# Performance work log

Measured on AMD Instinct MI355X. Metric: run time of the kernel, lower is better.

The kernel has to match this reference:

```python
import jax, jax.numpy as jnp
import numpy as np
from jax import lax
from jax.scipy.special import logsumexp

B, S, H, T, V = 64, 512, 768, 16, 30522


def setup_inputs() -> dict:
    key = jax.random.key(0)
    ks = jax.random.split(key, 8)
    src = jax.random.randint(ks[0], (B, S), 0, V, dtype=jnp.int32)
    label = jax.random.randint(ks[1], (B, S), 0, T, dtype=jnp.int32)
    padding_mask = jnp.ones((B, S), jnp.int32)
    emb_table = jax.random.normal(ks[2], (V, H), jnp.float32) * 0.02
    W = jax.random.normal(ks[3], (H, T), jnp.float32) * 0.02
    b = jnp.zeros((T,), jnp.float32)
    start_trans = jax.random.normal(ks[4], (T,), jnp.float32) * 0.1
    end_trans = jax.random.normal(ks[5], (T,), jnp.float32) * 0.1
    transitions = jax.random.normal(ks[6], (T, T), jnp.float32) * 0.1
    return dict(src=src, label=label, padding_mask=padding_mask,
                emb_table=emb_table, W=W, b=b, start_trans=start_trans,
                end_trans=end_trans, transitions=transitions)


def crf_log_likelihood(emissions, tags, mask, start_trans, end_trans, transitions):
    # emissions [S,B,T], tags [S,B] int, mask [S,B] float. torchcrf reduction='sum'.
    nS, nB, nT = emissions.shape
    barange = jnp.arange(nB)
    # --- numerator: score of the gold path ---
    score0 = start_trans[tags[0]] + emissions[0, barange, tags[0]]
    def num_step(score, xs):
        em_t, tag_prev, tag_t, m = xs
        s = transitions[tag_prev, tag_t] + em_t[barange, tag_t]
        return score + s * m, None
    num, _ = lax.scan(num_step, score0, (emissions[1:], tags[:-1], tags[1:], mask[1:]))
    seq_len = jnp.sum(mask, axis=0).astype(jnp.int32)          # [B]
    last_tags = tags[seq_len - 1, barange]
    num = num + end_trans[last_tags]
    # --- denominator: forward algorithm (per-step logsumexp) ---
    alpha0 = start_trans[None, :] + emissions[0]               # [B,T]
    def den_step(alpha, xs):
        em_t, m = xs
        nxt = logsumexp(alpha[:, :, None] + transitions[None, :, :] + em_t[:, None, :], axis=1)
        return jnp.where(m[:, None] > 0, nxt, alpha), None
    alpha, _ = lax.scan(den_step, alpha0, (emissions[1:], mask[1:]))
    den = logsumexp(alpha + end_trans[None, :], axis=1)
    return jnp.sum(num - den)


def viterbi_decode(emissions, start_trans, end_trans, transitions):
    # emissions [S,B,T]; full-length decode (no mask, as in the original call).
    score0 = start_trans[None, :] + emissions[0]               # [B,T]
    def fwd_step(score, em_t):
        br = score[:, :, None] + transitions[None, :, :] + em_t[:, None, :]  # [B,T,T]
        return jnp.max(br, axis=1), jnp.argmax(br, axis=1)
    score, hist = lax.scan(fwd_step, score0, emissions[1:])    # hist [S-1,B,T]
    last = jnp.argmax(score + end_trans[None, :], axis=1)      # [B]
    def back_step(tag, h_t):
        prev = jnp.take_along_axis(h_t, tag[:, None], axis=1)[:, 0]
        return prev, prev
    _, prevs = lax.scan(back_step, last, hist, reverse=True)   # prevs[t] = tag at t
    return jnp.concatenate([prevs, last[None, :]], axis=0)     # [S,B]


def reference(src, label, padding_mask, emb_table, W, b, start_trans, end_trans, transitions):
    bs = src.shape[0]
    emb = emb_table[src]                                       # [B,S,H]
    logits = jnp.einsum('bsh,ht->bst', emb, W) + b             # [B,S,T] (dropout in eval = identity)
    emissions = jnp.transpose(logits, (1, 0, 2))               # [S,B,T]
    tags = label.T                                             # [S,B]
    mask = padding_mask.T.astype(logits.dtype)                 # [S,B]
    ll = crf_log_likelihood(emissions, tags, mask, start_trans, end_trans, transitions)
    loss = -ll / bs
    predict = viterbi_decode(emissions, start_trans, end_trans, transitions).T  # [B,S]
    label_flat = label.reshape(-1)
    pred_flat = predict.reshape(-1).astype(label_flat.dtype)
    label_mask = (label_flat > 0).astype(label_flat.dtype)
    pred_flat = pred_flat * label_mask
    correct = jnp.sum((pred_flat == label_flat).astype(jnp.float32))
    return loss, correct, pred_flat, label_flat
```

## Files before the change

kernel.cpp:

```cpp
#include <hip/hip_runtime.h>

#define Bq 64
#define Sq 512
#define Hq 768
#define Tq 16
#define Vq 30522
#define EMP 516
#define WLP 20

typedef unsigned int u32;
typedef unsigned long long u64;
typedef unsigned char u8;

__device__ __forceinline__ float bperm_f(float v, int byteidx) {
    return __int_as_float(__builtin_amdgcn_ds_bpermute(byteidx, __float_as_int(v)));
}
template <int CTRL>
__device__ __forceinline__ int dpp_i(int v) {
    return __builtin_amdgcn_mov_dpp(v, CTRL, 0xF, 0xF, true);
}
template <int CTRL>
__device__ __forceinline__ float dpp_f(float v) {
    return __int_as_float(dpp_i<CTRL>(__float_as_int(v)));
}

#define QX1 0xB1
#define QX2 0x4E
#define QX3 0x1B
#define RR4  0x124
#define RR8  0x128
#define RR12 0x12C

__device__ __forceinline__ u32 packnib(u32 d) {
    u32 y = d | (d >> 4);
    y &= 0x00FF00FFu;
    y = (y | (y >> 8)) & 0xFFFFu;
    return y;
}
__device__ __forceinline__ u32 nib64(u64 f, u32 s) {
    return ((u32)(f >> (s << 2))) & 15u;
}

__global__ __launch_bounds__(256, 2) void k_table(const float* __restrict__ emb,
                                                  const float* __restrict__ W,
                                                  const float* __restrict__ bias,
                                                  float* __restrict__ table,
                                                  float* __restrict__ out) {
    if (blockIdx.x == 0 && threadIdx.x == 0) out[1] = 0.0f;
    __shared__ float WL[Hq * WLP];
    const int tid = threadIdx.x;

    #pragma unroll
    for (int k = 0; k < 12; ++k) {
        int idx = tid + (k << 8);
        float4 v = *reinterpret_cast<const float4*>(W + idx * 4);
        *reinterpret_cast<float4*>(&WL[(idx >> 2) * WLP + ((idx & 3) << 2)]) = v;
    }
    __syncthreads();

    const int r_loc = tid >> 2;
    const int q     = tid & 3;
    const int v     = blockIdx.x * 64 + r_loc;
    const int vc    = v < Vq ? v : Vq - 1;
    const float* arow = emb + (size_t)vc * Hq;

    float acc[16];
    #pragma unroll
    for (int t = 0; t < 16; ++t) acc[t] = 0.0f;

    float4 buf[8];
    #pragma unroll
    for (int u = 0; u < 8; ++u)
        buf[u] = *reinterpret_cast<const float4*>(arow + (q + 4 * u) * 4);

    for (int k6 = 0; k6 < 6; ++k6) {
        #pragma unroll
        for (int u = 0; u < 8; ++u) {
            const int k = k6 * 8 + u;
            float4 av = buf[u];
            if (k + 8 < 48)
                buf[u] = *reinterpret_cast<const float4*>(arow + (q + 4 * (k + 8)) * 4);
            const int hb = (q + 4 * k) * 4;
            #pragma unroll
            for (int a = 0; a < 4; ++a) {
                float s = (a == 0) ? av.x : (a == 1) ? av.y : (a == 2) ? av.z : av.w;
                const float* wr = &WL[(hb + a) * WLP];
                float4 w0 = *reinterpret_cast<const float4*>(wr);
                float4 w1 = *reinterpret_cast<const float4*>(wr + 4);
                float4 w2 = *reinterpret_cast<const float4*>(wr + 8);
                float4 w3 = *reinterpret_cast<const float4*>(wr + 12);
                acc[0]  = fmaf(s, w0.x, acc[0]);
                acc[1]  = fmaf(s, w0.y, acc[1]);
                acc[2]  = fmaf(s, w0.z, acc[2]);
                acc[3]  = fmaf(s, w0.w, acc[3]);
                acc[4]  = fmaf(s, w1.x, acc[4]);
                acc[5]  = fmaf(s, w1.y, acc[5]);
                acc[6]  = fmaf(s, w1.z, acc[6]);
                acc[7]  = fmaf(s, w1.w, acc[7]);
                acc[8]  = fmaf(s, w2.x, acc[8]);
                acc[9]  = fmaf(s, w2.y, acc[9]);
                acc[10] = fmaf(s, w2.z, acc[10]);
                acc[11] = fmaf(s, w2.w, acc[11]);
                acc[12] = fmaf(s, w3.x, acc[12]);
                acc[13] = fmaf(s, w3.y, acc[13]);
                acc[14] = fmaf(s, w3.z, acc[14]);
                acc[15] = fmaf(s, w3.w, acc[15]);
            }
        }
    }
    #pragma unroll
    for (int t = 0; t < 16; ++t) {
        acc[t] += dpp_f<QX1>(acc[t]);
        acc[t] += dpp_f<QX2>(acc[t]);
    }
    if (v < Vq) {
        float4 bv = *reinterpret_cast<const float4*>(bias + q * 4);
        float4 o = make_float4(acc[q * 4] + bv.x, acc[q * 4 + 1] + bv.y,
                               acc[q * 4 + 2] + bv.z, acc[q * 4 + 3] + bv.w);
        *reinterpret_cast<float4*>(table + (size_t)v * Tq + q * 4) = o;
    }
}

#define G16_DPP(PV) \
      float r1 = dpp_f<QX1>(PV), r2 = dpp_f<QX2>(PV), r3 = dpp_f<QX3>(PV); \
      float r4 = dpp_f<RR4>(PV), r8v = dpp_f<RR8>(PV), r12v = dpp_f<RR12>(PV); \
      float r5 = dpp_f<QX1>(r4), r6 = dpp_f<QX2>(r4), r7 = dpp_f<QX3>(r4); \
      float r9 = dpp_f<QX1>(r8v), r10 = dpp_f<QX2>(r8v), r11 = dpp_f<QX3>(r8v); \
      float r13 = dpp_f<QX1>(r12v), r14 = dpp_f<QX2>(r12v), r15 = dpp_f<QX3>(r12v);

#define G16_BP(PV) \
      const int rb_ = (lane & 48) << 2; \
      float r1 = bperm_f(PV, rb_ + (pm[1] << 2)),  r2 = bperm_f(PV, rb_ + (pm[2] << 2)); \
      float r3 = bperm_f(PV, rb_ + (pm[3] << 2)),  r4 = bperm_f(PV, rb_ + (pm[4] << 2)); \
      float r5 = bperm_f(PV, rb_ + (pm[5] << 2)),  r6 = bperm_f(PV, rb_ + (pm[6] << 2)); \
      float r7 = bperm_f(PV, rb_ + (pm[7] << 2)),  r8v = bperm_f(PV, rb_ + (pm[8] << 2)); \
      float r9 = bperm_f(PV, rb_ + (pm[9] << 2)),  r10 = bperm_f(PV, rb_ + (pm[10] << 2)); \
      float r11 = bperm_f(PV, rb_ + (pm[11] << 2)), r12v = bperm_f(PV, rb_ + (pm[12] << 2)); \
      float r13 = bperm_f(PV, rb_ + (pm[13] << 2)), r14 = bperm_f(PV, rb_ + (pm[14] << 2)); \
      float r15 = bperm_f(PV, rb_ + (pm[15] << 2));

#define DEN_BODY(ff) \
      float a0 = P * Wt[0];     a0 = fmaf(r1, Wt[1], a0);   a0 = fmaf(r2, Wt[2], a0);   a0 = fmaf(r3, Wt[3], a0); \
      float a1 = r4 * Wt[4];    a1 = fmaf(r5, Wt[5], a1);   a1 = fmaf(r6, Wt[6], a1);   a1 = fmaf(r7, Wt[7], a1); \
      float a2 = r8v * Wt[8];   a2 = fmaf(r9, Wt[9], a2);   a2 = fmaf(r10, Wt[10], a2); a2 = fmaf(r11, Wt[11], a2); \
      float a3 = r12v * Wt[12]; a3 = fmaf(r13, Wt[13], a3); a3 = fmaf(r14, Wt[14], a3); a3 = fmaf(r15, Wt[15], a3); \
      P = ((a0 + a1) + (a2 + a3)) * (ff);

#define DEN_STEP_F(ff) { G16_DPP(P); DEN_BODY(ff) }
#define DEN_STEP_B(ff) { G16_BP(P);  DEN_BODY(ff) }

#define VIT_BODY(emv, tcur) \
      float v0 = P + Wt[0],     v1 = r1 + Wt[1],    v2 = r2 + Wt[2],    v3 = r3 + Wt[3]; \
      float v4 = r4 + Wt[4],    v5 = r5 + Wt[5],    v6 = r6 + Wt[6],    v7 = r7 + Wt[7]; \
      float v8 = r8v + Wt[8],   v9 = r9 + Wt[9],    v10 = r10 + Wt[10], v11 = r11 + Wt[11]; \
      float v12 = r12v + Wt[12], v13 = r13 + Wt[13], v14 = r14 + Wt[14], v15 = r15 + Wt[15]; \
      float ma = fmaxf(fmaxf(v0, v1), v2),  mb = fmaxf(fmaxf(v3, v4), v5); \
      float mc = fmaxf(fmaxf(v6, v7), v8),  md = fmaxf(fmaxf(v9, v10), v11); \
      float me = fmaxf(fmaxf(v12, v13), v14); \
      float mv = fmaxf(fmaxf(fmaxf(ma, mb), mc), fmaxf(fmaxf(md, me), v15)); \
      P = mv + (emv); \
      if (lane < 16) scb[(tcur) * Tq + j] = P;

#define VIT_STEP_F(emv, tcur) { G16_DPP(P); VIT_BODY(emv, tcur) }
#define VIT_STEP_B(emv, tcur) { G16_BP(P);  VIT_BODY(emv, tcur) }

#define SCAN4(STEP, X1, X2, X3) \
      STEP(f0.X1, 1) STEP(f0.X2, 2) STEP(f0.X3, 3) \
      { float4 fc = emrow[1]; \
        for (int t0 = 4; t0 < Sq; t0 += 4) { \
            float4 fn; \
            if (t0 + 4 < Sq) fn = emrow[(t0 >> 2) + 1]; \
            STEP(fc.x, t0) STEP(fc.y, t0 + 1) STEP(fc.z, t0 + 2) STEP(fc.w, t0 + 3) \
            fc = fn; \
        } }

#define DSTEP_F(emv, tcur) DEN_STEP_F(emv)
#define DSTEP_B(emv, tcur) DEN_STEP_B(emv)

__global__ __launch_bounds__(64) void k_scan(const int* __restrict__ src,
                                             const int* __restrict__ label,
                                             const int* __restrict__ pmask,
                                             const float* __restrict__ table,
                                             const float* __restrict__ start_t,
                                             const float* __restrict__ end_t,
                                             const float* __restrict__ trans,
                                             float* __restrict__ nd,
                                             float* __restrict__ out) {
    __shared__ __align__(16) char smem[78848];

    const int lane = threadIdx.x;
    const int j  = lane & 15;
    const int b4 = lane >> 4;
    const bool vit = blockIdx.x >= 32;

    int pm[16];
    bool fast;
    {
        float x = __int_as_float(j);
        G16_DPP(x);
        pm[0] = j;
        pm[1] = __float_as_int(r1);   pm[2] = __float_as_int(r2);   pm[3] = __float_as_int(r3);
        pm[4] = __float_as_int(r4);   pm[5] = __float_as_int(r5);   pm[6] = __float_as_int(r6);
        pm[7] = __float_as_int(r7);   pm[8] = __float_as_int(r8v);  pm[9] = __float_as_int(r9);
        pm[10] = __float_as_int(r10); pm[11] = __float_as_int(r11); pm[12] = __float_as_int(r12v);
        pm[13] = __float_as_int(r13); pm[14] = __float_as_int(r14); pm[15] = __float_as_int(r15);
        u32 cov = 0;
        bool inr = true;
        #pragma unroll
        for (int s = 0; s < 16; ++s) {
            inr = inr && (pm[s] >= 0) && (pm[s] < 16);
            cov |= 1u << (pm[s] & 15);
        }
        fast = (__all((inr && cov == 0xFFFFu) ? 1 : 0) != 0);
        if (!fast) {
            pm[0] = j;
            #pragma unroll
            for (int s = 1; s < 16; ++s) pm[s] = (j + s) & 15;
        }
    }

    if (!vit) {
        float* emT = (float*)smem;
        int* srcl  = (int*)(smem + 66048);
        int* labl  = (int*)(smem + 70144);
        const int bb = blockIdx.x * 2;
        const int bm = b4 & 1;
        const int batch = bb + bm;

        #pragma unroll
        for (int k = 0; k < 16; ++k) {
            int idx = lane + (k << 6);
            int bch = idx >> 9, t = idx & 511;
            srcl[idx] = src[(bb + bch) * Sq + t];
            labl[idx] = label[(bb + bch) * Sq + t];
        }
        __syncthreads();
        #pragma unroll 4
        for (int k = 0; k < 256; ++k) {
            int idx = lane + (k << 6);
            int bch = idx >> 13, rem = idx & 8191;
            int t = rem >> 4, jj = rem & 15;
            emT[(bch * 16 + jj) * EMP + t] =
                __expf(table[(size_t)srcl[(bch << 9) + t] * Tq + jj]) * 0.0625f;
        }
        __syncthreads();

        float Wt[16];
        #pragma unroll
        for (int s = 0; s < 16; ++s) Wt[s] = __expf(trans[pm[s] * Tq + j]);

        const float4* emrow = reinterpret_cast<const float4*>(emT + (bm * 16 + j) * EMP);
        float4 f0 = emrow[0];
        float P = __expf(start_t[j]) * f0.x * 16.0f;
        float* scb = nullptr; (void)scb;

        if (fast) { SCAN4(DSTEP_F, y, z, w) }
        else      { SCAN4(DSTEP_B, y, z, w) }

        float val = P * __expf(end_t[j]);
        val += dpp_f<QX1>(val); val += dpp_f<QX2>(val);
        val += dpp_f<RR4>(val); val += dpp_f<RR8>(val);
        float den = (float)(511.0 * 2.7725887222397811) + __logf(val);

        float numv = 0.0f;
        int sl = 0;
        #pragma unroll
        for (int k = 0; k < 32; ++k) {
            int t = j + (k << 4);
            int tag = labl[(bm << 9) + t];
            int m = pmask[batch * Sq + t];
            sl += m;
            float emtt = table[(size_t)srcl[(bm << 9) + t] * Tq + tag];
            if (t == 0) {
                numv += start_t[tag] + emtt;
            } else {
                int tp = labl[(bm << 9) + t - 1];
                numv += (float)m * (trans[tp * Tq + tag] + emtt);
            }
        }
        numv += dpp_f<QX1>(numv); numv += dpp_f<QX2>(numv);
        numv += dpp_f<RR4>(numv); numv += dpp_f<RR8>(numv);
        sl += dpp_i<QX1>(sl); sl += dpp_i<QX2>(sl);
        sl += dpp_i<RR4>(sl); sl += dpp_i<RR8>(sl);
        if (j == 0 && b4 < 2) {
            int last = labl[(bm << 9) + sl - 1];
            nd[batch] = (numv + end_t[last]) - den;
        }
    } else {
        float* em   = (float*)smem;
        float* scb  = (float*)(smem + 33024);
        u8*  hist   = (u8*)(smem + 65792);
        int* srcl   = (int*)(smem + 73984);
        int* labl   = (int*)(smem + 76032);
        u8*  predi  = (u8*)(smem + 78080);
        const int batch = blockIdx.x - 32;

        #pragma unroll
        for (int k = 0; k < 8; ++k) {
            int t = lane + (k << 6);
            srcl[t] = src[batch * Sq + t];
            labl[t] = label[batch * Sq + t];
        }
        __syncthreads();
        #pragma unroll 4
        for (int k = 0; k < 128; ++k) {
            int idx = lane + (k << 6);
            int t = idx >> 4, jj = idx & 15;
            em[jj * EMP + t] = table[(size_t)srcl[t] * Tq + jj];
        }
        __syncthreads();

        float Wt[16];
        #pragma unroll
        for (int s = 0; s < 16; ++s) Wt[s] = trans[pm[s] * Tq + j];

        const float4* emrow = reinterpret_cast<const float4*>(em + j * EMP);
        float4 f0 = emrow[0];
        float P = start_t[j] + f0.x;
        if (lane < 16) scb[j] = P;

        if (fast) { SCAN4(VIT_STEP_F, y, z, w) }
        else      { SCAN4(VIT_STEP_B, y, z, w) }

        float fv = P + end_t[j];
        int fi = j;
        #pragma unroll
        for (int off = 1; off < 16; off <<= 1) {
            float ov = __shfl_xor(fv, off);
            int oi = __shfl_xor(fi, off);
            bool take = (ov > fv) || (ov == fv && oi < fi);
            fv = take ? ov : fv;
            fi = take ? oi : fi;
        }
        __syncthreads();

        {
            float Tt[16];
            #pragma unroll
            for (int m = 0; m < 16; ++m) Tt[m] = trans[m * Tq + j];
            const int r = b4;
            for (int k = 0; k < 128; ++k) {
                int t = 1 + r + 4 * k;
                if (t < Sq) {
                    const float4* sr = reinterpret_cast<const float4*>(scb + (t - 1) * Tq);
                    float4 s0 = sr[0], s1 = sr[1], s2 = sr[2], s3 = sr[3];
                    float w0 = s0.x + Tt[0],  w1 = s0.y + Tt[1],  w2 = s0.z + Tt[2],  w3 = s0.w + Tt[3];
                    float w4 = s1.x + Tt[4],  w5 = s1.y + Tt[5],  w6 = s1.z + Tt[6],  w7 = s1.w + Tt[7];
                    float w8 = s2.x + Tt[8],  w9 = s2.y + Tt[9],  wA = s2.z + Tt[10], wB = s2.w + Tt[11];
                    float wC = s3.x + Tt[12], wD = s3.y + Tt[13], wE = s3.z + Tt[14], wF = s3.w + Tt[15];
                    float ma = fmaxf(fmaxf(w0, w1), w2),  mb = fmaxf(fmaxf(w3, w4), w5);
                    float mc = fmaxf(fmaxf(w6, w7), w8),  md = fmaxf(fmaxf(w9, wA), wB);
                    float me = fmaxf(fmaxf(wC, wD), wE);
                    float mv = fmaxf(fmaxf(fmaxf(ma, mb), mc), fmaxf(fmaxf(md, me), wF));
                    float y0 = fmaf(mv - w0, 1e30f, 0.0f),  y1 = fmaf(mv - w1, 1e30f, 1.0f);
                    float y2 = fmaf(mv - w2, 1e30f, 2.0f),  y3 = fmaf(mv - w3, 1e30f, 3.0f);
                    float y4 = fmaf(mv - w4, 1e30f, 4.0f),  y5 = fmaf(mv - w5, 1e30f, 5.0f);
                    float y6 = fmaf(mv - w6, 1e30f, 6.0f),  y7 = fmaf(mv - w7, 1e30f, 7.0f);
                    float y8 = fmaf(mv - w8, 1e30f, 8.0f),  y9 = fmaf(mv - w9, 1e30f, 9.0f);
                    float yA = fmaf(mv - wA, 1e30f, 10.0f), yB = fmaf(mv - wB, 1e30f, 11.0f);
                    float yC = fmaf(mv - wC, 1e30f, 12.0f), yD = fmaf(mv - wD, 1e30f, 13.0f);
                    float yE = fmaf(mv - wE, 1e30f, 14.0f), yF = fmaf(mv - wF, 1e30f, 15.0f);
                    float na = fminf(fminf(y0, y1), y2),  nb = fminf(fminf(y3, y4), y5);
                    float nc = fminf(fminf(y6, y7), y8),  nd2 = fminf(fminf(y9, yA), yB);
                    float ne = fminf(fminf(yC, yD), yE);
                    float ym = fminf(fminf(fminf(na, nb), nc), fminf(fminf(nd2, ne), yF));
                    hist[(t - 1) * Tq + j] = (unsigned char)(int)ym;
                }
            }
        }
        if (lane < 16) hist[511 * Tq + lane] = (u8)lane;
        __syncthreads();

        u64 rp[8];
        #pragma unroll
        for (int k = 0; k < 8; ++k) {
            uint4 rw = *reinterpret_cast<const uint4*>(&hist[(lane * 8 + k) * Tq]);
            u32 lo = packnib(rw.x) | (packnib(rw.y) << 16);
            u32 hi = packnib(rw.z) | (packnib(rw.w) << 16);
            rp[k] = (u64)lo | ((u64)hi << 32);
        }
        u64 F = rp[7];
        #pragma unroll
        for (int k = 6; k >= 0; --k) {
            u64 nf = 0;
            #pragma unroll
            for (int e = 0; e < 16; ++e) {
                u32 s = (u32)(F >> (e * 4)) & 15u;
                nf |= ((u64)nib64(rp[k], s)) << (e * 4);
            }
            F = nf;
        }
        u32 Flo = (u32)F, Fhi = (u32)(F >> 32);

        u32 pk[8] = {0, 0, 0, 0, 0, 0, 0, 0};
        u32 E = (u32)__builtin_amdgcn_readlane(fi, 0) & 15u;
        #pragma unroll 64
        for (int c = 63; c >= 0; --c) {
            u64 Fc = ((u64)(u32)__builtin_amdgcn_readlane((int)Fhi, c) << 32)
                   | (u64)(u32)__builtin_amdgcn_readlane((int)Flo, c);
            pk[c >> 3] |= E << ((c & 7) * 4);
            E = nib64(Fc, E);
        }

        u32 a0s = (lane & 8) ? pk[1] : pk[0];
        u32 a1s = (lane & 8) ? pk[3] : pk[2];
        u32 a2s = (lane & 8) ? pk[5] : pk[4];
        u32 a3s = (lane & 8) ? pk[7] : pk[6];
        u32 b0s = (lane & 16) ? a1s : a0s;
        u32 b1s = (lane & 16) ? a3s : a2s;
        u32 c0s = (lane & 32) ? b1s : b0s;
        u32 cur = (c0s >> ((lane & 7) * 4)) & 15u;
        u32 w0 = 0, w1 = 0;
        #pragma unroll
        for (int k = 7; k >= 0; --k) {
            cur = nib64(rp[k], cur);
            if (k >= 4) w1 |= cur << ((k - 4) * 8);
            else        w0 |= cur << (k * 8);
        }
        *reinterpret_cast<uint2*>(&predi[lane * 8]) = make_uint2(w0, w1);
        __syncthreads();

        int cnt = 0;
        #pragma unroll
        for (int k = 0; k < 8; ++k) {
            int s_ = lane + (k << 6);
            int lab = labl[s_];
            int pr = (int)predi[s_];
            int mpr = lab > 0 ? pr : 0;
            out[2 + batch * Sq + s_] = (float)mpr;
            out[2 + Bq * Sq + batch * Sq + s_] = (float)lab;
            cnt += (mpr == lab) ? 1 : 0;
        }
        #pragma unroll
        for (int off = 1; off < 64; off <<= 1) cnt += __shfl_xor(cnt, off);
        if (lane == 0) atomicAdd(out + 1, (float)cnt);
    }
}

__global__ __launch_bounds__(64) void k_final(const float* __restrict__ nd,
                                              float* __restrict__ out) {
    float v = nd[threadIdx.x];
    #pragma unroll
    for (int off = 1; off < 64; off <<= 1) v += __shfl_xor(v, off);
    if (threadIdx.x == 0) out[0] = -v * (1.0f / (float)Bq);
}

extern "C" void kernel_launch(void* const* d_in, const int* in_sizes, int n_in,
                              void* d_out, int out_size, void* d_ws, size_t ws_size,
                              hipStream_t stream) {
    const int*   src   = (const int*)d_in[0];
    const int*   label = (const int*)d_in[1];
    const int*   pmask = (const int*)d_in[2];
    const float* emb   = (const float*)d_in[3];
    const float* W     = (const float*)d_in[4];
    const float* bias  = (const float*)d_in[5];
    const float* st    = (const float*)d_in[6];
    const float* en    = (const float*)d_in[7];
    const float* tr    = (const float*)d_in[8];
    float* out = (float*)d_out;

    float* table = (float*)d_ws;
    float* nd    = table + (size_t)Vq * Tq;

    const int nblk = (Vq + 63) / 64;
    k_table<<<nblk, 256, 0, stream>>>(emb, W, bias, table, out);
    k_scan<<<96, 64, 0, stream>>>(src, label, pmask, table, st, en, tr, nd, out);
    k_final<<<1, 64, 0, stream>>>(nd, out);
}
```

Before: 97.46 us.

## Use row-rotate DPP gathers, batch Viterbi score stores, drop final reduction kernel

Builds the 16-lane gather from single row_ror DPP moves instead of chained quad-permute plus rotate, which shortens the dependency chain of each serial scan step. Viterbi scores are kept in registers for four steps and written with one spread store per group instead of a lane-masked store every step. The separate final reduction kernel is removed: each batch's loss contribution is atomically added to the output, which saves a launch at the cost of a nondeterministic float summation order. The scan loops are rewritten explicitly with unroll 2.

```diff
diff --git a/kernel.cpp b/kernel.cpp
--- a/kernel.cpp
+++ b/kernel.cpp
@@ -23,13 +23,15 @@
 __device__ __forceinline__ float dpp_f(float v) {
     return __int_as_float(dpp_i<CTRL>(__float_as_int(v)));
 }
+template <int N>
+__device__ __forceinline__ float ror_f(float v) {
+    return __int_as_float(__builtin_amdgcn_mov_dpp(__float_as_int(v), 0x120 + N, 0xF, 0xF, true));
+}
 
 #define QX1 0xB1
 #define QX2 0x4E
-#define QX3 0x1B
 #define RR4  0x124
 #define RR8  0x128
-#define RR12 0x12C
 
 __device__ __forceinline__ u32 packnib(u32 d) {
     u32 y = d | (d >> 4);
@@ -46,7 +48,7 @@
                                                   const float* __restrict__ bias,
                                                   float* __restrict__ table,
                                                   float* __restrict__ out) {
-    if (blockIdx.x == 0 && threadIdx.x == 0) out[1] = 0.0f;
+    if (blockIdx.x == 0 && threadIdx.x == 0) { out[0] = 0.0f; out[1] = 0.0f; }
     __shared__ float WL[Hq * WLP];
     const int tid = threadIdx.x;
 
@@ -121,12 +123,12 @@
     }
 }
 
-#define G16_DPP(PV) \
-      float r1 = dpp_f<QX1>(PV), r2 = dpp_f<QX2>(PV), r3 = dpp_f<QX3>(PV); \
-      float r4 = dpp_f<RR4>(PV), r8v = dpp_f<RR8>(PV), r12v = dpp_f<RR12>(PV); \
-      float r5 = dpp_f<QX1>(r4), r6 = dpp_f<QX2>(r4), r7 = dpp_f<QX3>(r4); \
-      float r9 = dpp_f<QX1>(r8v), r10 = dpp_f<QX2>(r8v), r11 = dpp_f<QX3>(r8v); \
-      float r13 = dpp_f<QX1>(r12v), r14 = dpp_f<QX2>(r12v), r15 = dpp_f<QX3>(r12v);
+#define G16_ROR(PV) \
+      float r1 = ror_f<1>(PV),  r2 = ror_f<2>(PV),  r3 = ror_f<3>(PV); \
+      float r4 = ror_f<4>(PV),  r5 = ror_f<5>(PV),  r6 = ror_f<6>(PV); \
+      float r7 = ror_f<7>(PV),  r8v = ror_f<8>(PV), r9 = ror_f<9>(PV); \
+      float r10 = ror_f<10>(PV), r11 = ror_f<11>(PV), r12v = ror_f<12>(PV); \
+      float r13 = ror_f<13>(PV), r14 = ror_f<14>(PV), r15 = ror_f<15>(PV);
 
 #define G16_BP(PV) \
       const int rb_ = (lane & 48) << 2; \
@@ -146,36 +148,27 @@
       float a3 = r12v * Wt[12]; a3 = fmaf(r13, Wt[13], a3); a3 = fmaf(r14, Wt[14], a3); a3 = fmaf(r15, Wt[15], a3); \
       P = ((a0 + a1) + (a2 + a3)) * (ff);
 
-#define DEN_STEP_F(ff) { G16_DPP(P); DEN_BODY(ff) }
-#define DEN_STEP_B(ff) { G16_BP(P);  DEN_BODY(ff) }
-
-#define VIT_BODY(emv, tcur) \
+#define DSTEP_F(ff) { G16_ROR(P); DEN_BODY(ff) }
+#define DSTEP_B(ff) { G16_BP(P);  DEN_BODY(ff) }
+
+#define VIT_BODY(emv) \
       float v0 = P + Wt[0],     v1 = r1 + Wt[1],    v2 = r2 + Wt[2],    v3 = r3 + Wt[3]; \
       float v4 = r4 + Wt[4],    v5 = r5 + Wt[5],    v6 = r6 + Wt[6],    v7 = r7 + Wt[7]; \
       float v8 = r8v + Wt[8],   v9 = r9 + Wt[9],    v10 = r10 + Wt[10], v11 = r11 + Wt[11]; \
       float v12 = r12v + Wt[12], v13 = r13 + Wt[13], v14 = r14 + Wt[14], v15 = r15 + Wt[15]; \
-      float ma = fmaxf(fmaxf(v0, v1), v2),  mb = fmaxf(fmaxf(v3, v4), v5); \
-      float mc = fmaxf(fmaxf(v6, v7), v8),  md = fmaxf(fmaxf(v9, v10), v11); \
-      float me = fmaxf(fmaxf(v12, v13), v14); \
-      float mv = fmaxf(fmaxf(fmaxf(ma, mb), mc), fmaxf(fmaxf(md, me), v15)); \
-      P = mv + (emv); \
-      if (lane < 16) scb[(tcur) * Tq + j] = P;
-
-#define VIT_STEP_F(emv, tcur) { G16_DPP(P); VIT_BODY(emv, tcur) }
-#define VIT_STEP_B(emv, tcur) { G16_BP(P);  VIT_BODY(emv, tcur) }
-
-#define SCAN4(STEP, X1, X2, X3) \
-      STEP(f0.X1, 1) STEP(f0.X2, 2) STEP(f0.X3, 3) \
-      { float4 fc = emrow[1]; \
-        for (int t0 = 4; t0 < Sq; t0 += 4) { \
-            float4 fn; \
-            if (t0 + 4 < Sq) fn = emrow[(t0 >> 2) + 1]; \
-            STEP(fc.x, t0) STEP(fc.y, t0 + 1) STEP(fc.z, t0 + 2) STEP(fc.w, t0 + 3) \
-            fc = fn; \
-        } }
-
-#define DSTEP_F(emv, tcur) DEN_STEP_F(emv)
-#define DSTEP_B(emv, tcur) DEN_STEP_B(emv)
+      float m0 = fmaxf(fmaxf(v0, v1), v2),   m1 = fmaxf(fmaxf(v3, v4), v5); \
+      float m2 = fmaxf(fmaxf(v6, v7), v8),   m3 = fmaxf(fmaxf(v9, v10), v11); \
+      float m4 = fmaxf(fmaxf(v12, v13), v14); \
+      float mA = fmaxf(fmaxf(m0, m1), m2),   mB = fmaxf(fmaxf(m3, m4), v15); \
+      P = fmaxf(mA, mB) + (emv);
+
+#define VSTEP_F(emv) { G16_ROR(P); VIT_BODY(emv) }
+#define VSTEP_B(emv) { G16_BP(P);  VIT_BODY(emv) }
+
+#define VGSTORE(t0) { \
+      float s01 = (b4 & 1) ? S1 : S0; \
+      float s23 = (b4 & 1) ? S3 : S2; \
+      scb[((t0) + b4) * Tq + j] = (b4 & 2) ? s23 : s01; }
 
 __global__ __launch_bounds__(64) void k_scan(const int* __restrict__ src,
                                              const int* __restrict__ label,
@@ -184,7 +177,6 @@
                                              const float* __restrict__ start_t,
                                              const float* __restrict__ end_t,
                                              const float* __restrict__ trans,
-                                             float* __restrict__ nd,
                                              float* __restrict__ out) {
     __shared__ __align__(16) char smem[78848];
 
@@ -197,7 +189,7 @@
     bool fast;
     {
         float x = __int_as_float(j);
-        G16_DPP(x);
+        G16_ROR(x);
         pm[0] = j;
         pm[1] = __float_as_int(r1);   pm[2] = __float_as_int(r2);   pm[3] = __float_as_int(r3);
         pm[4] = __float_as_int(r4);   pm[5] = __float_as_int(r5);   pm[6] = __float_as_int(r6);
@@ -252,11 +244,26 @@
         const float4* emrow = reinterpret_cast<const float4*>(emT + (bm * 16 + j) * EMP);
         float4 f0 = emrow[0];
         float P = __expf(start_t[j]) * f0.x * 16.0f;
-        float* scb = nullptr; (void)scb;
-
-        if (fast) { SCAN4(DSTEP_F, y, z, w) }
-        else      { SCAN4(DSTEP_B, y, z, w) }
-
+
+        if (fast) {
+            DSTEP_F(f0.y) DSTEP_F(f0.z) DSTEP_F(f0.w)
+            float4 fc = emrow[1];
+            #pragma unroll 2
+            for (int g = 1; g < 128; ++g) {
+                float4 fn = emrow[g + 1];
+                DSTEP_F(fc.x) DSTEP_F(fc.y) DSTEP_F(fc.z) DSTEP_F(fc.w)
+                fc = fn;
+            }
+        } else {
+            DSTEP_B(f0.y) DSTEP_B(f0.z) DSTEP_B(f0.w)
+            float4 fc = emrow[1];
+            #pragma unroll 2
+            for (int g = 1; g < 128; ++g) {
+                float4 fn = emrow[g + 1];
+                DSTEP_B(fc.x) DSTEP_B(fc.y) DSTEP_B(fc.z) DSTEP_B(fc.w)
+                fc = fn;
+            }
+        }
         float val = P * __expf(end_t[j]);
         val += dpp_f<QX1>(val); val += dpp_f<QX2>(val);
         val += dpp_f<RR4>(val); val += dpp_f<RR8>(val);
@@ -284,7 +291,8 @@
         sl += dpp_i<RR4>(sl); sl += dpp_i<RR8>(sl);
         if (j == 0 && b4 < 2) {
             int last = labl[(bm << 9) + sl - 1];
-            nd[batch] = (numv + end_t[last]) - den;
+            float v = (numv + end_t[last]) - den;
+            atomicAdd(out, -v * (1.0f / (float)Bq));
         }
     } else {
         float* em   = (float*)smem;
@@ -317,10 +325,42 @@
         const float4* emrow = reinterpret_cast<const float4*>(em + j * EMP);
         float4 f0 = emrow[0];
         float P = start_t[j] + f0.x;
-        if (lane < 16) scb[j] = P;
-
-        if (fast) { SCAN4(VIT_STEP_F, y, z, w) }
-        else      { SCAN4(VIT_STEP_B, y, z, w) }
+
+        if (fast) {
+            float S0 = P;
+            VSTEP_F(f0.y) float S1 = P;
+            VSTEP_F(f0.z) float S2 = P;
+            VSTEP_F(f0.w) float S3 = P;
+            VGSTORE(0)
+            float4 fc = emrow[1];
+            #pragma unroll 2
+            for (int g = 1; g < 128; ++g) {
+                float4 fn = emrow[g + 1];
+                VSTEP_F(fc.x) S0 = P;
+                VSTEP_F(fc.y) S1 = P;
+                VSTEP_F(fc.z) S2 = P;
+                VSTEP_F(fc.w) S3 = P;
+                VGSTORE(g * 4)
+                fc = fn;
+            }
+        } else {
+            float S0 = P;
+            VSTEP_B(f0.y) float S1 = P;
+            VSTEP_B(f0.z) float S2 = P;
+            VSTEP_B(f0.w) float S3 = P;
+            VGSTORE(0)
+            float4 fc = emrow[1];
+            #pragma unroll 2
+            for (int g = 1; g < 128; ++g) {
+                float4 fn = emrow[g + 1];
+                VSTEP_B(fc.x) S0 = P;
+                VSTEP_B(fc.y) S1 = P;
+                VSTEP_B(fc.z) S2 = P;
+                VSTEP_B(fc.w) S3 = P;
+                VGSTORE(g * 4)
+                fc = fn;
+            }
+        }
 
         float fv = P + end_t[j];
         int fi = j;
@@ -437,14 +477,6 @@
     }
 }
 
-__global__ __launch_bounds__(64) void k_final(const float* __restrict__ nd,
-                                              float* __restrict__ out) {
-    float v = nd[threadIdx.x];
-    #pragma unroll
-    for (int off = 1; off < 64; off <<= 1) v += __shfl_xor(v, off);
-    if (threadIdx.x == 0) out[0] = -v * (1.0f / (float)Bq);
-}
-
 extern "C" void kernel_launch(void* const* d_in, const int* in_sizes, int n_in,
                               void* d_out, int out_size, void* d_ws, size_t ws_size,
                               hipStream_t stream) {
@@ -460,10 +492,8 @@
     float* out = (float*)d_out;
 
     float* table = (float*)d_ws;
-    float* nd    = table + (size_t)Vq * Tq;
 
     const int nblk = (Vq + 63) / 64;
     k_table<<<nblk, 256, 0, stream>>>(emb, W, bias, table, out);
-    k_scan<<<96, 64, 0, stream>>>(src, label, pmask, table, st, en, tr, nd, out);
-    k_final<<<1, 64, 0, stream>>>(nd, out);
-}
+    k_scan<<<96, 64, 0, stream>>>(src, label, pmask, table, st, en, tr, out);
+}
```

Result: faster. 91.60 us (-6.0%).
